# Kernel tuning notes

Measured on AMD Instinct MI355X. Metric: run time of the kernel, lower is better.

Reference implementation:

```python
import jax, jax.numpy as jnp
import numpy as np

WBITS = 4   # weight bits (symmetric signed)
ABITS = 4   # activation bits (unsigned, [0,1])
CBITS = 4   # partial-sum quantization bits
ARRAY = 128 # crossbar array size (input-dim tile)
BN_EPS = 1e-5


def ste_round(x):
    # straight-through estimator round (identity gradient)
    return x + jax.lax.stop_gradient(jnp.round(x) - x)


def setup_inputs() -> dict:
    key = jax.random.key(0)
    k1, k2 = jax.random.split(key)
    B, FIN, FOUT = 65536, 256, 256
    x = jax.random.uniform(k1, (B, FIN), dtype=jnp.float32)        # quantized-act range [0,1]
    weight = jax.random.normal(k2, (FOUT, FIN), dtype=jnp.float32) * 0.05
    gamma = jnp.ones((FOUT,), jnp.float32)
    beta = jnp.zeros((FOUT,), jnp.float32)
    return {"x": x, "weight": weight, "gamma": gamma, "beta": beta}


def reference(x, weight, gamma, beta):
    qmax_w = 2 ** (WBITS - 1) - 1          # 7
    qmax_a = 2 ** ABITS - 1                # 15

    # --- symmetric weight quantization to WBITS (integer levels) ---
    scale_w = jnp.max(jnp.abs(weight)) / qmax_w
    w_int = ste_round(jnp.clip(weight / scale_w, -qmax_w, qmax_w))  # [Fout, Fin]

    # --- unsigned activation quantization to ABITS (integer levels) ---
    x_int = ste_round(jnp.clip(x, 0.0, 1.0) * qmax_a)               # [B, Fin]

    # --- crossbar-tiled integer matmul with partial-sum quantization ---
    B, Fin = x.shape
    Fout = weight.shape[0]
    T = Fin // ARRAY
    xt = x_int.reshape(B, T, ARRAY)          # [B, T, A]
    wt = w_int.reshape(Fout, T, ARRAY)       # [Fout, T, A]
    psum = jnp.einsum('bta,ota->bto', xt, wt)  # integer partial sums, [B, T, Fout]

    # quantize each partial sum to CBITS levels over the full tile dynamic range
    pmax = float(ARRAY * qmax_a * qmax_w)
    step = (2.0 * pmax) / (2 ** CBITS - 1)
    psum_q = ste_round(psum / step) * step

    acc = psum_q.sum(axis=1) * (scale_w / qmax_a)   # dequantized linear output [B, Fout]

    # --- BatchNorm1d (training mode: batch statistics) ---
    mu = acc.mean(axis=0)
    var = acc.var(axis=0)
    y = (acc - mu) * jax.lax.rsqrt(var + BN_EPS) * gamma + beta

    # --- quantized clipped-ReLU activation to ABITS ---
    out = ste_round(jnp.clip(y, 0.0, 1.0) * qmax_a) / qmax_a
    return out
```

## Files before the change

kernel.cpp:

```cpp
#include <hip/hip_runtime.h>
#include <cstdint>
#include <cstddef>

typedef int   v4i __attribute__((ext_vector_type(4)));
typedef float v4f __attribute__((ext_vector_type(4)));

static constexpr int NREP = 8;

static constexpr size_t WQ_OFF    = 0;
static constexpr size_t STATS_OFF = 65536;
static constexpr size_t PART_OFF  = STATS_OFF + NREP*512*4;
static constexpr size_t SBUF_OFF  = 131072 + 2048;
static constexpr size_t WS_NEEDED = SBUF_OFF + (size_t)65536 * 256;

__device__ __forceinline__ int rhe1792(int p) {
    unsigned u = (unsigned)(p + 17024);
    unsigned v = u >> 8;
    unsigned d = (v * 147u) >> 10;
    int q = (int)d - 9;
    unsigned tie = (unsigned)(((u & 255u) | (v - 7u * d)) == 0u);
    q -= (int)(tie & ((unsigned)q & 1u));
    return q;
}

__global__ void k_maxabs(const float* __restrict__ w, float* __restrict__ partials,
                         int* __restrict__ stats) {
    __shared__ float wmax[4];
    int idx = blockIdx.x * 256 + threadIdx.x;
    float4 f = ((const float4*)w)[idx];
    float m = fmaxf(fmaxf(fabsf(f.x), fabsf(f.y)), fmaxf(fabsf(f.z), fabsf(f.w)));
    #pragma unroll
    for (int s = 32; s > 0; s >>= 1) m = fmaxf(m, __shfl_xor(m, s, 64));
    if ((threadIdx.x & 63) == 0) wmax[threadIdx.x >> 6] = m;
    if (idx < NREP * 512) stats[idx] = 0;
    __syncthreads();
    if (threadIdx.x == 0)
        partials[blockIdx.x] = fmaxf(fmaxf(wmax[0], wmax[1]), fmaxf(wmax[2], wmax[3]));
}

__device__ __forceinline__ float reduce_partials(const float* __restrict__ partials, int tid) {
    float p = partials[tid & 63];
    #pragma unroll
    for (int s = 32; s > 0; s >>= 1) p = fmaxf(p, __shfl_xor(p, s, 64));
    return p;
}

__global__ void k_wquant(const float* __restrict__ w, const float* __restrict__ partials,
                         signed char* __restrict__ wq) {
    int idx = blockIdx.x * 256 + threadIdx.x;
    float scale = reduce_partials(partials, threadIdx.x) / 7.0f;
    float4 f = ((const float4*)w)[idx];
    int q0 = (int)rintf(fminf(fmaxf(f.x / scale, -7.f), 7.f));
    int q1 = (int)rintf(fminf(fmaxf(f.y / scale, -7.f), 7.f));
    int q2 = (int)rintf(fminf(fmaxf(f.z / scale, -7.f), 7.f));
    int q3 = (int)rintf(fminf(fmaxf(f.w / scale, -7.f), 7.f));
    ((int*)wq)[idx] = (q0 & 255) | ((q1 & 255) << 8) | ((q2 & 255) << 16) | ((q3 & 255) << 24);
}

template <typename ST>
__global__ __launch_bounds__(512, 1) void k_gemm(
    const float* __restrict__ x, const signed char* __restrict__ wq,
    ST* __restrict__ sbuf, int* __restrict__ stats)
{
    __shared__ __align__(16) signed char ldsx[64 * 272];
    const int tid  = threadIdx.x;
    const int lane = tid & 63;
    const int wv   = tid >> 6;
    const int obase = wv * 32;
    const int lr = lane & 15, quad = lane >> 4;
    const size_t rb0 = (size_t)blockIdx.x * 64;

    v4i wf[2][4];
    #pragma unroll
    for (int ot = 0; ot < 2; ++ot)
        #pragma unroll
        for (int kt = 0; kt < 4; ++kt)
            wf[ot][kt] = *(const v4i*)(wq + (size_t)(obase + ot * 16 + lr) * 256 + kt * 64 + quad * 16);

    const v4f* xb = (const v4f*)(x + rb0 * 256);
    #pragma unroll
    for (int p = 0; p < 2; ++p) {
        v4f f[4];
        #pragma unroll
        for (int j = 0; j < 4; ++j)
            f[j] = xb[p * 2048 + j * 512 + tid];
        #pragma unroll
        for (int j = 0; j < 4; ++j) {
            int idx = p * 2048 + j * 512 + tid;
            int row = idx >> 6, c = idx & 63;
            int b0 = (int)rintf(fminf(fmaxf(f[j][0], 0.f), 1.f) * 15.f);
            int b1 = (int)rintf(fminf(fmaxf(f[j][1], 0.f), 1.f) * 15.f);
            int b2 = (int)rintf(fminf(fmaxf(f[j][2], 0.f), 1.f) * 15.f);
            int b3 = (int)rintf(fminf(fmaxf(f[j][3], 0.f), 1.f) * 15.f);
            *(int*)(ldsx + row * 272 + c * 4) = b0 | (b1 << 8) | (b2 << 16) | (b3 << 24);
        }
    }
    __syncthreads();

    int ssum[2] = {0, 0};
    int ssq[2]  = {0, 0};

    #pragma unroll
    for (int t = 0; t < 4; ++t) {
        v4i a[4];
        #pragma unroll
        for (int kt = 0; kt < 4; ++kt)
            a[kt] = *(const v4i*)(ldsx + (t * 16 + lr) * 272 + kt * 64 + quad * 16);
        #pragma unroll
        for (int ot = 0; ot < 2; ++ot) {
            v4i acc0 = {0, 0, 0, 0}, acc1 = {0, 0, 0, 0};
            acc0 = __builtin_amdgcn_mfma_i32_16x16x64_i8(a[0], wf[ot][0], acc0, 0, 0, 0);
            acc0 = __builtin_amdgcn_mfma_i32_16x16x64_i8(a[1], wf[ot][1], acc0, 0, 0, 0);
            acc1 = __builtin_amdgcn_mfma_i32_16x16x64_i8(a[2], wf[ot][2], acc1, 0, 0, 0);
            acc1 = __builtin_amdgcn_mfma_i32_16x16x64_i8(a[3], wf[ot][3], acc1, 0, 0, 0);
            const int ocol = obase + ot * 16 + lr;
            if constexpr (sizeof(ST) == 1) {
                unsigned pack = 0;
                #pragma unroll
                for (int e = 0; e < 4; ++e) {
                    int s = rhe1792(acc0[e]) + rhe1792(acc1[e]);
                    ssum[ot] += s;
                    ssq[ot]  += s * s;
                    pack |= (unsigned)(s & 255) << (8 * e);
                }
                const size_t rg = (size_t)blockIdx.x * 16 + t * 4 + quad;
                ((unsigned*)sbuf)[rg * 256 + ocol] = pack;
            } else {
                ST* sp = sbuf + (rb0 + (size_t)t * 16 + quad * 4) * 256 + ocol;
                #pragma unroll
                for (int e = 0; e < 4; ++e) {
                    int s = rhe1792(acc0[e]) + rhe1792(acc1[e]);
                    ssum[ot] += s;
                    ssq[ot]  += s * s;
                    sp[(size_t)e * 256] = (ST)s;
                }
            }
        }
    }
    int* st = stats + (blockIdx.x & (NREP - 1)) * 512;
    #pragma unroll
    for (int ot = 0; ot < 2; ++ot) {
        int v = ssum[ot], u = ssq[ot];
        v += __shfl_xor(v, 16, 64); v += __shfl_xor(v, 32, 64);
        u += __shfl_xor(u, 16, 64); u += __shfl_xor(u, 32, 64);
        if (quad == 0) {
            atomicAdd(&st[obase + ot * 16 + lr], v);
            atomicAdd(&st[256 + obase + ot * 16 + lr], u);
        }
    }
}

template <typename LT>
__global__ __launch_bounds__(256) void k_out(const LT* sbuf, const int* __restrict__ stats,
                                             const float* __restrict__ partials,
                                             const float* __restrict__ gamma,
                                             const float* __restrict__ beta,
                                             float* out)
{
    __shared__ float2 ab[256];
    const int tid = threadIdx.x;
    {
        int o = tid;
        int s = 0, q = 0;
        #pragma unroll
        for (int rr = 0; rr < NREP; ++rr) {
            s += stats[rr * 512 + o];
            q += stats[rr * 512 + 256 + o];
        }
        float scale_w = reduce_partials(partials, o) / 7.0f;
        float t = scale_w / 15.0f;
        double Cs = 1792.0 * (double)t;
        const double N = 65536.0;
        double mean_s = (double)s / N;
        double var_s  = (double)q / N - mean_s * mean_s;
        double var    = Cs * Cs * var_s;
        double inv    = 1.0 / sqrt(var + 1e-5);
        double A = Cs * inv * (double)gamma[o];
        double B = (double)beta[o] - Cs * mean_s * inv * (double)gamma[o];
        ab[o] = make_float2((float)A, (float)B);
    }
    __syncthreads();

    const int b = blockIdx.x;
    const int d = ((b & 7) << 2) | ((b >> 3) & 3) | (b & ~31);
    const int ci = tid & 63;
    const int c0 = ci * 4;
    const float2 p0 = ab[c0], p1 = ab[c0 + 1], p2 = ab[c0 + 2], p3 = ab[c0 + 3];
    const float inv15 = 0.066666666666666666f;

    if constexpr (sizeof(LT) == 1) {
        const int rg = d * 4 + (tid >> 6);
        v4i V = ((const v4i*)sbuf)[(size_t)rg * 64 + ci];
        #pragma unroll
        for (int j = 0; j < 4; ++j) {
            float v0 = (float)((V[0] << (24 - 8 * j)) >> 24);
            float v1 = (float)((V[1] << (24 - 8 * j)) >> 24);
            float v2 = (float)((V[2] << (24 - 8 * j)) >> 24);
            float v3 = (float)((V[3] << (24 - 8 * j)) >> 24);
            float y0 = rintf(fminf(fmaxf(v0 * p0.x + p0.y, 0.f), 1.f) * 15.f);
            float y1 = rintf(fminf(fmaxf(v1 * p1.x + p1.y, 0.f), 1.f) * 15.f);
            float y2 = rintf(fminf(fmaxf(v2 * p2.x + p2.y, 0.f), 1.f) * 15.f);
            float y3 = rintf(fminf(fmaxf(v3 * p3.x + p3.y, 0.f), 1.f) * 15.f);
            v4f o = { y0 * inv15, y1 * inv15, y2 * inv15, y3 * inv15 };
            __builtin_nontemporal_store(o, (v4f*)out + (size_t)(4 * rg + j) * 64 + ci);
        }
    } else {
        const size_t base = (size_t)d * 1024 + tid;
        #pragma unroll
        for (int j = 0; j < 4; ++j) {
            const size_t F4 = base + (size_t)j * 256;
            v4f fl = ((const v4f*)sbuf)[F4];
            const int oo = (tid * 4) & 255;
            float2 q0 = ab[oo], q1 = ab[oo + 1], q2 = ab[oo + 2], q3 = ab[oo + 3];
            float y0 = rintf(fminf(fmaxf(fl[0] * q0.x + q0.y, 0.f), 1.f) * 15.f);
            float y1 = rintf(fminf(fmaxf(fl[1] * q1.x + q1.y, 0.f), 1.f) * 15.f);
            float y2 = rintf(fminf(fmaxf(fl[2] * q2.x + q2.y, 0.f), 1.f) * 15.f);
            float y3 = rintf(fminf(fmaxf(fl[3] * q3.x + q3.y, 0.f), 1.f) * 15.f);
            v4f o = { y0 * inv15, y1 * inv15, y2 * inv15, y3 * inv15 };
            __builtin_nontemporal_store(o, (v4f*)out + F4);
        }
    }
}

extern "C" void kernel_launch(void* const* d_in, const int* in_sizes, int n_in,
                              void* d_out, int out_size, void* d_ws, size_t ws_size,
                              hipStream_t stream)
{
    const float* x     = (const float*)d_in[0];
    const float* w     = (const float*)d_in[1];
    const float* gamma = (const float*)d_in[2];
    const float* beta  = (const float*)d_in[3];
    float* out = (float*)d_out;
    char* ws = (char*)d_ws;

    signed char* wq       = (signed char*)(ws + WQ_OFF);
    int*         stats    = (int*)(ws + STATS_OFF);
    float*       partials = (float*)(ws + PART_OFF);

    k_maxabs<<<dim3(64), dim3(256), 0, stream>>>(w, partials, stats);
    k_wquant<<<dim3(64), dim3(256), 0, stream>>>(w, partials, wq);

    if (ws_size >= WS_NEEDED) {
        signed char* sbuf = (signed char*)(ws + SBUF_OFF);
        k_gemm<signed char><<<dim3(1024), dim3(512), 0, stream>>>(x, wq, sbuf, stats);
        k_out<signed char><<<dim3(4096), dim3(256), 0, stream>>>(sbuf, stats, partials,
                                                                 gamma, beta, out);
    } else {
        k_gemm<float><<<dim3(1024), dim3(512), 0, stream>>>(x, wq, out, stats);
        k_out<float><<<dim3(4096), dim3(256), 0, stream>>>(out, stats, partials,
                                                           gamma, beta, out);
    }
}
```

Before: 131.3 us.

## Double GEMM rows per block and compute BN coefficients in last-finishing block

Each GEMM block now processes 128 rows instead of 64, halving the grid to 512 blocks so the per-wave weight fragments are reused over more rows and fewer atomics hit the stats buffer. A done-counter with a last-block pattern computes the BatchNorm scale/shift table once in the GEMM kernel. The output kernel then just loads the precomputed table instead of having every block redundantly reduce stats in double precision. This costs doubled LDS per block and a serial tail in the last GEMM block, and 512 blocks may underfill the GPU's compute units.

```diff
diff --git a/kernel.cpp b/kernel.cpp
--- a/kernel.cpp
+++ b/kernel.cpp
@@ -10,6 +10,8 @@
 static constexpr size_t WQ_OFF    = 0;
 static constexpr size_t STATS_OFF = 65536;
 static constexpr size_t PART_OFF  = STATS_OFF + NREP*512*4;
+static constexpr size_t DONE_OFF  = PART_OFF + 64*4;
+static constexpr size_t ABTAB_OFF = DONE_OFF + 64;
 static constexpr size_t SBUF_OFF  = 131072 + 2048;
 static constexpr size_t WS_NEEDED = SBUF_OFF + (size_t)65536 * 256;
 
@@ -24,7 +26,7 @@
 }
 
 __global__ void k_maxabs(const float* __restrict__ w, float* __restrict__ partials,
-                         int* __restrict__ stats) {
+                         int* __restrict__ stats, int* __restrict__ done) {
     __shared__ float wmax[4];
     int idx = blockIdx.x * 256 + threadIdx.x;
     float4 f = ((const float4*)w)[idx];
@@ -33,6 +35,7 @@
     for (int s = 32; s > 0; s >>= 1) m = fmaxf(m, __shfl_xor(m, s, 64));
     if ((threadIdx.x & 63) == 0) wmax[threadIdx.x >> 6] = m;
     if (idx < NREP * 512) stats[idx] = 0;
+    if (idx == 0) *done = 0;
     __syncthreads();
     if (threadIdx.x == 0)
         partials[blockIdx.x] = fmaxf(fmaxf(wmax[0], wmax[1]), fmaxf(wmax[2], wmax[3]));
@@ -60,15 +63,19 @@
 template <typename ST>
 __global__ __launch_bounds__(512, 1) void k_gemm(
     const float* __restrict__ x, const signed char* __restrict__ wq,
-    ST* __restrict__ sbuf, int* __restrict__ stats)
+    ST* __restrict__ sbuf, int* __restrict__ stats,
+    int* __restrict__ done, float2* __restrict__ abtab,
+    const float* __restrict__ partials,
+    const float* __restrict__ gamma, const float* __restrict__ beta)
 {
-    __shared__ __align__(16) signed char ldsx[64 * 272];
+    __shared__ __align__(16) signed char ldsx[128 * 272];
+    __shared__ int lastflag;
     const int tid  = threadIdx.x;
     const int lane = tid & 63;
     const int wv   = tid >> 6;
     const int obase = wv * 32;
     const int lr = lane & 15, quad = lane >> 4;
-    const size_t rb0 = (size_t)blockIdx.x * 64;
+    const size_t rb0 = (size_t)blockIdx.x * 128;
 
     v4i wf[2][4];
     #pragma unroll
@@ -79,7 +86,7 @@
 
     const v4f* xb = (const v4f*)(x + rb0 * 256);
     #pragma unroll
-    for (int p = 0; p < 2; ++p) {
+    for (int p = 0; p < 4; ++p) {
         v4f f[4];
         #pragma unroll
         for (int j = 0; j < 4; ++j)
@@ -101,7 +108,7 @@
     int ssq[2]  = {0, 0};
 
     #pragma unroll
-    for (int t = 0; t < 4; ++t) {
+    for (int t = 0; t < 8; ++t) {
         v4i a[4];
         #pragma unroll
         for (int kt = 0; kt < 4; ++kt)
@@ -123,7 +130,7 @@
                     ssq[ot]  += s * s;
                     pack |= (unsigned)(s & 255) << (8 * e);
                 }
-                const size_t rg = (size_t)blockIdx.x * 16 + t * 4 + quad;
+                const size_t rg = (size_t)blockIdx.x * 32 + t * 4 + quad;
                 ((unsigned*)sbuf)[rg * 256 + ocol] = pack;
             } else {
                 ST* sp = sbuf + (rb0 + (size_t)t * 16 + quad * 4) * 256 + ocol;
@@ -148,24 +155,22 @@
             atomicAdd(&st[256 + obase + ot * 16 + lr], u);
         }
     }
-}
-
-template <typename LT>
-__global__ __launch_bounds__(256) void k_out(const LT* sbuf, const int* __restrict__ stats,
-                                             const float* __restrict__ partials,
-                                             const float* __restrict__ gamma,
-                                             const float* __restrict__ beta,
-                                             float* out)
-{
-    __shared__ float2 ab[256];
-    const int tid = threadIdx.x;
-    {
-        int o = tid;
+
+    __syncthreads();
+    if (tid == 0) {
+        __threadfence();
+        int old = atomicAdd(done, 1);
+        lastflag = (old == (int)gridDim.x - 1);
+    }
+    __syncthreads();
+    if (lastflag && tid < 256) {
+        __threadfence();
+        const int o = tid;
         int s = 0, q = 0;
         #pragma unroll
         for (int rr = 0; rr < NREP; ++rr) {
-            s += stats[rr * 512 + o];
-            q += stats[rr * 512 + 256 + o];
+            s += __hip_atomic_load(&stats[rr * 512 + o],       __ATOMIC_RELAXED, __HIP_MEMORY_SCOPE_AGENT);
+            q += __hip_atomic_load(&stats[rr * 512 + 256 + o], __ATOMIC_RELAXED, __HIP_MEMORY_SCOPE_AGENT);
         }
         float scale_w = reduce_partials(partials, o) / 7.0f;
         float t = scale_w / 15.0f;
@@ -177,8 +182,18 @@
         double inv    = 1.0 / sqrt(var + 1e-5);
         double A = Cs * inv * (double)gamma[o];
         double B = (double)beta[o] - Cs * mean_s * inv * (double)gamma[o];
-        ab[o] = make_float2((float)A, (float)B);
-    }
+        abtab[o] = make_float2((float)A, (float)B);
+    }
+}
+
+template <typename LT>
+__global__ __launch_bounds__(256) void k_out(const LT* sbuf,
+                                             const float2* __restrict__ abtab,
+                                             float* out)
+{
+    __shared__ float2 ab[256];
+    const int tid = threadIdx.x;
+    ab[tid] = abtab[tid];
     __syncthreads();
 
     const int b = blockIdx.x;
@@ -236,18 +251,22 @@
     signed char* wq       = (signed char*)(ws + WQ_OFF);
     int*         stats    = (int*)(ws + STATS_OFF);
     float*       partials = (float*)(ws + PART_OFF);
-
-    k_maxabs<<<dim3(64), dim3(256), 0, stream>>>(w, partials, stats);
+    int*         done     = (int*)(ws + DONE_OFF);
+    float2*      abtab    = (float2*)(ws + ABTAB_OFF);
+
+    k_maxabs<<<dim3(64), dim3(256), 0, stream>>>(w, partials, stats, done);
     k_wquant<<<dim3(64), dim3(256), 0, stream>>>(w, partials, wq);
 
     if (ws_size >= WS_NEEDED) {
         signed char* sbuf = (signed char*)(ws + SBUF_OFF);
-        k_gemm<signed char><<<dim3(1024), dim3(512), 0, stream>>>(x, wq, sbuf, stats);
-        k_out<signed char><<<dim3(4096), dim3(256), 0, stream>>>(sbuf, stats, partials,
-                                                                 gamma, beta, out);
+        k_gemm<signed char><<<dim3(512), dim3(512), 0, stream>>>(x, wq, sbuf, stats,
+                                                                 done, abtab, partials,
+                                                                 gamma, beta);
+        k_out<signed char><<<dim3(4096), dim3(256), 0, stream>>>(sbuf, abtab, out);
     } else {
-        k_gemm<float><<<dim3(1024), dim3(512), 0, stream>>>(x, wq, out, stats);
-        k_out<float><<<dim3(4096), dim3(256), 0, stream>>>(out, stats, partials,
-                                                           gamma, beta, out);
-    }
-}
+        k_gemm<float><<<dim3(512), dim3(512), 0, stream>>>(x, wq, out, stats,
+                                                           done, abtab, partials,
+                                                           gamma, beta);
+        k_out<float><<<dim3(4096), dim3(256), 0, stream>>>(out, abtab, out);
+    }
+}
```

New measurement: 152.7 us. +16.3%, slower.
